# Kernel tuning notes

Hardware: AMD Instinct MI355X
Metric: run time of the kernel (lower is better)

## Reference

```python
import jax, jax.numpy as jnp
import numpy as np

H = 8
D_MODEL = 1024
D_K = D_MODEL // H
NEG = -1000000000.0


def layer_norm(x, a, b, eps=1e-06):
    # torch std: unbiased (ddof=1); module divides by (std + eps)
    mean = jnp.mean(x, axis=-1, keepdims=True)
    var = jnp.sum((x - mean) ** 2, axis=-1, keepdims=True) / (x.shape[-1] - 1)
    std = jnp.sqrt(var)
    return a * (x - mean) / (std + eps) + b


def setup_inputs() -> dict:
    key = jax.random.key(0)
    ks = jax.random.split(key, 12)
    B, S, D = 8, 1024, D_MODEL
    inp = {
        "query": jax.random.normal(ks[0], (B, S, D), jnp.float32),
        "value": jax.random.normal(ks[1], (B, S, D), jnp.float32),
        "key": jax.random.normal(ks[2], (B, S, D), jnp.float32),
        "mask": jax.random.randint(ks[3], (B, S), 0, 2, jnp.int32),
        "ln_a": jnp.ones((D,), jnp.float32),
        "ln_b": jnp.zeros((D,), jnp.float32),
        "wq": jax.random.normal(ks[4], (D, D), jnp.float32) * 0.02,
        "bq": jnp.zeros((D,), jnp.float32),
        "wk": jax.random.normal(ks[5], (D, D), jnp.float32) * 0.02,
        "bk": jnp.zeros((D,), jnp.float32),
        "wv": jax.random.normal(ks[6], (D, D), jnp.float32) * 0.02,
        "bv": jnp.zeros((D,), jnp.float32),
        "w_aoa": jax.random.normal(ks[7], (2 * D, 2 * D), jnp.float32) * 0.02,  # [out, in]
        "b_aoa": jnp.zeros((2 * D,), jnp.float32),
    }
    return inp


def reference(query, value, key, mask, ln_a, ln_b, wq, bq, wk, bk, wv, bv, w_aoa, b_aoa):
    B, S, D = query.shape
    # mask [B,S] -> [B,1,1,S]
    m = mask[:, None, None, :]
    # norm_q
    q = layer_norm(query, ln_a, ln_b)
    # QKV projections, split heads -> [B,H,S,Dk]
    def split_heads(x):
        return x.reshape(B, -1, H, D_K).transpose(0, 2, 1, 3)
    q_ = split_heads(q @ wq.T + bq)
    k_ = split_heads(key @ wk.T + bk)
    v_ = split_heads(value @ wv.T + bv)
    scores = jnp.einsum("bhqd,bhkd->bhqk", q_, k_) / jnp.sqrt(jnp.float32(D_K))
    scores = jnp.where(m == 0, NEG, scores)
    p = jax.nn.softmax(scores, axis=-1)
    x = jnp.einsum("bhqk,bhkd->bhqd", p, v_)
    x = x.transpose(0, 2, 1, 3).reshape(B, S, D)
    # AoA: concat with (normed) query, linear to 2D, GLU
    z = jnp.concatenate([x, q], axis=-1) @ w_aoa.T + b_aoa
    a, g = jnp.split(z, 2, axis=-1)
    return a * jax.nn.sigmoid(g)
```

## Files before the change

### kernel.cpp

```cpp
#include <hip/hip_runtime.h>

typedef __attribute__((ext_vector_type(8))) __bf16 bf16x8;
typedef __attribute__((ext_vector_type(4))) float f32x4;

__device__ __forceinline__ ushort f2b(float f) {
    uint u = __builtin_bit_cast(uint, f);
    u += 0x7fffu + ((u >> 16) & 1u);
    return (ushort)(u >> 16);
}
__device__ __forceinline__ float b2f(ushort h) {
    uint u = ((uint)h) << 16;
    return __builtin_bit_cast(float, u);
}

__global__ __launch_bounds__(256) void cast_kernel(const float* __restrict__ src,
                                                   ushort* __restrict__ dst) {
    size_t i = ((size_t)blockIdx.x * 256 + threadIdx.x) * 4;
    float4 v = *(const float4*)(src + i);
    ushort4 o;
    o.x = f2b(v.x); o.y = f2b(v.y); o.z = f2b(v.z); o.w = f2b(v.w);
    *(ushort4*)(dst + i) = o;
}

__global__ __launch_bounds__(256) void ln_kernel(const float* __restrict__ x,
                                                 const float* __restrict__ ga,
                                                 const float* __restrict__ be,
                                                 ushort* __restrict__ xq) {
    const int row = blockIdx.x, tid = threadIdx.x;
    __shared__ float red[4];
    float4 v = ((const float4*)(x + (size_t)row * 1024))[tid];
    float sm = v.x + v.y + v.z + v.w;
    for (int off = 32; off; off >>= 1) sm += __shfl_xor(sm, off);
    if ((tid & 63) == 0) red[tid >> 6] = sm;
    __syncthreads();
    float mean = (red[0] + red[1] + red[2] + red[3]) * (1.f / 1024.f);
    __syncthreads();
    float dx = v.x - mean, dy = v.y - mean, dz = v.z - mean, dw = v.w - mean;
    float s2 = dx * dx + dy * dy + dz * dz + dw * dw;
    for (int off = 32; off; off >>= 1) s2 += __shfl_xor(s2, off);
    if ((tid & 63) == 0) red[tid >> 6] = s2;
    __syncthreads();
    float var = (red[0] + red[1] + red[2] + red[3]) * (1.f / 1023.f);
    float inv = 1.f / (sqrtf(var) + 1e-6f);
    float4 g = ((const float4*)ga)[tid];
    float4 bb = ((const float4*)be)[tid];
    ushort4 o;
    o.x = f2b(g.x * dx * inv + bb.x);
    o.y = f2b(g.y * dy * inv + bb.y);
    o.z = f2b(g.z * dz * inv + bb.z);
    o.w = f2b(g.w * dw * inv + bb.w);
    *(ushort4*)&xq[(size_t)row * 2048 + 1024 + tid * 4] = o;
}

__global__ __launch_bounds__(256) void gemm2(const ushort* __restrict__ A, int lda,
                                             const ushort* __restrict__ B, int ldb,
                                             const float* __restrict__ bias,
                                             ushort* __restrict__ C, int ldc,
                                             int K, int NB, float scale, int mode) {
    __shared__ ushort As[2][8192];
    __shared__ ushort Bs[2][8192];
    const int tid = threadIdx.x;
    const int w = tid >> 6, l = tid & 63;
    const int wr = w >> 1, wc = w & 1;
    const int r16 = l & 15, g4 = l >> 4;

    const int bid = blockIdx.x;
    const int cpx = gridDim.x >> 3;
    const int swz = (bid & 7) * cpx + (bid >> 3);
    const int m0 = (swz / NB) * 128;
    const int n0 = (swz % NB) * 128;

    const int srow = l >> 3;
    const int scol = ((l & 7) ^ srow) * 8;
    const ushort* Asrc = A + (size_t)(m0 + w * 8 + srow) * lda + scol;
    const ushort* Bsrc = B + (size_t)(n0 + w * 8 + srow) * ldb + scol;

    f32x4 acc[4][4];
#pragma unroll
    for (int i = 0; i < 4; i++)
#pragma unroll
        for (int j = 0; j < 4; j++) acc[i][j] = (f32x4){0.f, 0.f, 0.f, 0.f};

    auto STAGE = [&](int sel, int kt) {
#pragma unroll
        for (int it = 0; it < 4; it++) {
            __builtin_amdgcn_global_load_lds(
                (const __attribute__((address_space(1))) void*)(Asrc + (size_t)(it * 32) * lda + kt * 64),
                (__attribute__((address_space(3))) void*)(&As[sel][(it * 4 + w) * 512]), 16, 0, 0);
            __builtin_amdgcn_global_load_lds(
                (const __attribute__((address_space(1))) void*)(Bsrc + (size_t)(it * 32) * ldb + kt * 64),
                (__attribute__((address_space(3))) void*)(&Bs[sel][(it * 4 + w) * 512]), 16, 0, 0);
        }
    };

    const int swzr = (g4 ^ (r16 & 7)) << 4;

    auto COMPUTE = [&](int sel, int kt, bool stage_next) {
        if (stage_next) STAGE(sel ^ 1, kt + 1);
        const char* Ab = (const char*)&As[sel][0];
        const char* Bb = (const char*)&Bs[sel][0];
        bf16x8 af[4][2], bfv[4][2];
#pragma unroll
        for (int mi = 0; mi < 4; mi++) {
            int ba = (wr * 64 + mi * 16 + r16) * 128 + swzr;
            af[mi][0] = *(const bf16x8*)(Ab + ba);
            af[mi][1] = *(const bf16x8*)(Ab + (ba ^ 64));
        }
#pragma unroll
        for (int ni = 0; ni < 4; ni++) {
            int bb = (wc * 64 + ni * 16 + r16) * 128 + swzr;
            bfv[ni][0] = *(const bf16x8*)(Bb + bb);
            bfv[ni][1] = *(const bf16x8*)(Bb + (bb ^ 64));
        }
        __builtin_amdgcn_s_setprio(1);
#pragma unroll
        for (int ks = 0; ks < 2; ks++)
#pragma unroll
            for (int mi = 0; mi < 4; mi++)
#pragma unroll
                for (int ni = 0; ni < 4; ni++)
                    acc[mi][ni] = __builtin_amdgcn_mfma_f32_16x16x32_bf16(af[mi][ks], bfv[ni][ks], acc[mi][ni], 0, 0, 0);
        __builtin_amdgcn_s_setprio(0);
        asm volatile("s_waitcnt vmcnt(0)" ::: "memory");
        __syncthreads();
    };

    STAGE(0, 0);
    asm volatile("s_waitcnt vmcnt(0)" ::: "memory");
    __syncthreads();
    const int NT = K >> 6;
    for (int kt = 0; kt < NT; kt += 2) {
        COMPUTE(0, kt, true);
        COMPUTE(1, kt + 1, kt + 2 < NT);
    }

    const int row0 = m0 + wr * 64;
    const int col0 = n0 + wc * 64;
    if (mode == 0) {
#pragma unroll
        for (int ni = 0; ni < 4; ni++) {
            int n = col0 + ni * 16 + r16;
            float bs = bias[n];
#pragma unroll
            for (int mi = 0; mi < 4; mi++) {
                int mr = row0 + mi * 16 + g4 * 4;
#pragma unroll
                for (int r = 0; r < 4; r++) {
                    C[(size_t)(mr + r) * ldc + n] = f2b((acc[mi][ni][r] + bs) * scale);
                }
            }
        }
    } else {
#pragma unroll
        for (int ni = 0; ni < 4; ni++) {
            int n = col0 + ni * 16 + r16;
            float bs = bias[n];
            int h = n >> 7, d = n & 127;
#pragma unroll
            for (int mi = 0; mi < 4; mi++) {
                int m = row0 + mi * 16 + g4 * 4;
                int b_ = m >> 10, s_ = m & 1023;
                ushort4 o;
                o.x = f2b((acc[mi][ni][0] + bs) * scale);
                o.y = f2b((acc[mi][ni][1] + bs) * scale);
                o.z = f2b((acc[mi][ni][2] + bs) * scale);
                o.w = f2b((acc[mi][ni][3] + bs) * scale);
                *(ushort4*)&C[((size_t)(b_ * 8 + h) * 128 + d) * 1024 + s_] = o;
            }
        }
    }
}

__global__ __launch_bounds__(512, 2) void gemm3(const ushort* __restrict__ A, int lda,
                                                const ushort* __restrict__ B, int ldb,
                                                const float* __restrict__ bias,
                                                ushort* __restrict__ C, int ldc,
                                                int K, int NB) {
    __shared__ ushort lds[2][32768];

    const int tid = threadIdx.x;
    const int w = tid >> 6, l = tid & 63;
    const int wr = w >> 2, wcn = w & 3;
    const int r16 = l & 15, g4 = l >> 4;

    const int bid = blockIdx.x;
    const int cpx = gridDim.x >> 3;
    const int swz = (bid & 7) * cpx + (bid >> 3);
    const int m0 = (swz / NB) * 256;
    const int n0 = (swz % NB) * 256;

    const int srow8 = l >> 3;
    const int sxor8 = ((l & 7) ^ srow8) * 8;
    const ushort* As0 = A + (size_t)(m0 + w * 8 + srow8) * lda + sxor8;
    const ushort* Bs0 = B + (size_t)(n0 + w * 8 + srow8) * ldb + sxor8;

    f32x4 acc[8][4];
#pragma unroll
    for (int i = 0; i < 8; i++)
#pragma unroll
        for (int j = 0; j < 4; j++) acc[i][j] = (f32x4){0.f, 0.f, 0.f, 0.f};

    const int sw16 = (r16 & 7) << 4;
    char* ldsb = (char*)&lds[0][0];

#define STAGE_H(sel_, HS_, kt_)                                                            \
    do {                                                                                   \
        const int mat_ = (HS_)&1, half_ = (HS_) >> 1;                                      \
        const ushort* sb_ = mat_ ? Bs0 : As0;                                              \
        const int ld_ = mat_ ? ldb : lda;                                                  \
        _Pragma("unroll") for (int li_ = 0; li_ < 2; li_++) {                              \
            const ushort* src_ = sb_ + (size_t)(half_ * 128 + li_ * 64) * ld_ + (kt_)*64;  \
            int dst_ = (sel_)*65536 + mat_ * 32768 + half_ * 16384 + li_ * 8192 + w * 1024;\
            __builtin_amdgcn_global_load_lds(                                              \
                (const __attribute__((address_space(1))) void*)src_,                       \
                (__attribute__((address_space(3))) void*)(ldsb + dst_), 16, 0, 0);         \
        }                                                                                  \
    } while (0)

#define RD_A(sel_, a_, ks_)                                                                  \
    (*(const bf16x8*)(ldsb + (sel_)*65536 + ((a_) >> 2) * 16384 +                            \
                      (wr * 16 + 32 * ((a_)&3) + r16) * 128 + (((ks_)*64 + g4 * 16) ^ sw16)))
#define RD_B(sel_, b_, ks_)                                                                  \
    (*(const bf16x8*)(ldsb + (sel_)*65536 + 32768 + ((b_) >> 1) * 16384 +                    \
                      (wcn * 16 + 64 * ((b_)&1) + r16) * 128 + (((ks_)*64 + g4 * 16) ^ sw16)))

    const int NT = K >> 6;

    STAGE_H(0, 0, 0); STAGE_H(0, 1, 0); STAGE_H(0, 2, 0); STAGE_H(0, 3, 0);
    asm volatile("s_waitcnt vmcnt(0)" ::: "memory");
    __builtin_amdgcn_s_barrier();

    bf16x8 afr[4][2], bfr[2][2];

#define PHASE(sel_, t_, A0_, B0_, RDA_, RDB_, HS_)                                          \
    do {                                                                                    \
        if (RDA_) {                                                                         \
            _Pragma("unroll") for (int ai_ = 0; ai_ < 4; ai_++)                             \
                _Pragma("unroll") for (int ks_ = 0; ks_ < 2; ks_++)                         \
                    afr[ai_][ks_] = RD_A(sel_, (A0_) + ai_, ks_);                           \
        }                                                                                   \
        if (RDB_) {                                                                         \
            _Pragma("unroll") for (int bi_ = 0; bi_ < 2; bi_++)                             \
                _Pragma("unroll") for (int ks_ = 0; ks_ < 2; ks_++)                         \
                    bfr[bi_][ks_] = RD_B(sel_, (B0_) + bi_, ks_);                           \
        }                                                                                   \
        if ((t_) + 1 < NT) STAGE_H((sel_) ^ 1, HS_, (t_) + 1);                              \
        __builtin_amdgcn_s_barrier();                                                       \
        __builtin_amdgcn_s_setprio(1);                                                      \
        _Pragma("unroll") for (int ks_ = 0; ks_ < 2; ks_++)                                 \
            _Pragma("unroll") for (int ai_ = 0; ai_ < 4; ai_++)                             \
                _Pragma("unroll") for (int bi_ = 0; bi_ < 2; bi_++)                         \
                    acc[(A0_) + ai_][(B0_) + bi_] = __builtin_amdgcn_mfma_f32_16x16x32_bf16(\
                        afr[ai_][ks_], bfr[bi_][ks_], acc[(A0_) + ai_][(B0_) + bi_], 0, 0, 0);\
        __builtin_amdgcn_s_setprio(0);                                                      \
        asm volatile("s_waitcnt vmcnt(4)" ::: "memory");                                    \
        __builtin_amdgcn_s_barrier();                                                       \
    } while (0)

    for (int t = 0; t < NT; ++t) {
        const int sel = t & 1;
        PHASE(sel, t, 0, 0, 1, 1, 0);
        PHASE(sel, t, 4, 0, 1, 0, 1);
        PHASE(sel, t, 4, 2, 0, 1, 2);
        PHASE(sel, t, 0, 2, 1, 0, 3);
    }
#undef PHASE
#undef RD_A
#undef RD_B
#undef STAGE_H

#pragma unroll
    for (int b_ = 0; b_ < 4; b_++) {
        int n = n0 + wcn * 16 + 64 * b_ + r16;
        float bs = bias[n];
#pragma unroll
        for (int a_ = 0; a_ < 8; a_++) {
            int mr = m0 + wr * 16 + 32 * a_ + g4 * 4;
#pragma unroll
            for (int r = 0; r < 4; r++) {
                C[(size_t)(mr + r) * ldc + n] = f2b(acc[a_][b_][r] + bs);
            }
        }
    }
}

__global__ __launch_bounds__(512, 4) void attn_kernel(const ushort* __restrict__ Q,
                                                      const ushort* __restrict__ Kt,
                                                      const ushort* __restrict__ Vt,
                                                      const int* __restrict__ mask,
                                                      ushort* __restrict__ xq) {
    __shared__ ushort Ks[2][8192];
    __shared__ ushort Vs[2][8192];
    __shared__ ushort Pl[8][1024];

    const int tid = threadIdx.x;
    const int l = tid & 63, wid = tid >> 6;
    const int r16 = l & 15, g4 = l >> 4;
    const int id = blockIdx.x;
    const int bh = ((id >> 6) << 3) | (id & 7);
    const int qb = (id >> 3) & 7;
    const int b = bh >> 3, h = bh & 7;
    const int q0 = qb * 128 + wid * 16;

    bf16x8 qf[4];
    const ushort* Qrow = Q + (size_t)(b * 1024 + q0 + r16) * 1024 + h * 128 + g4 * 8;
#pragma unroll
    for (int kf = 0; kf < 4; kf++) qf[kf] = *(const bf16x8*)(Qrow + kf * 32);

    const ushort* Kg = Kt + ((size_t)b * 1024) * 1024 + h * 128;
    const ushort* Vg = Vt + (size_t)(b * 8 + h) * 128 * 1024;
    const int* mptr = mask + b * 1024;
    int mv = mptr[l];

    f32x4 xacc[8];
#pragma unroll
    for (int i = 0; i < 8; i++) xacc[i] = (f32x4){0.f, 0.f, 0.f, 0.f};
    float mrow = -INFINITY, lrow = 0.f;

    char* Pme = (char*)&Pl[wid][0];
    const int pswz = (r16 & 7) << 4;

    auto STAGE = [&](int sel, int t) {
        const int kv0 = t * 64;
#pragma unroll
        for (int it = 0; it < 2; ++it) {
            int ob = it * 8192 + wid * 1024;
            int o = ob + l * 16;
            int row = o >> 8;
            int sc = (o & 255) ^ ((row & 7) << 4);
            const ushort* src = Kg + (size_t)(kv0 + row) * 1024 + (sc >> 1);
            __builtin_amdgcn_global_load_lds((const __attribute__((address_space(1))) void*)src,
                (__attribute__((address_space(3))) void*)((char*)&Ks[sel][0] + ob), 16, 0, 0);
        }
#pragma unroll
        for (int it = 0; it < 2; ++it) {
            int ob = it * 8192 + wid * 1024;
            int o = ob + l * 16;
            int d = o >> 7;
            int sc = (o & 127) ^ ((d & 7) << 4);
            const ushort* src = Vg + (size_t)d * 1024 + kv0 + (sc >> 1);
            __builtin_amdgcn_global_load_lds((const __attribute__((address_space(1))) void*)src,
                (__attribute__((address_space(3))) void*)((char*)&Vs[sel][0] + ob), 16, 0, 0);
        }
    };

    STAGE(0, 0);
    int cur = 0;

    for (int t = 0; t < 16; ++t) {
        int mvn = (t < 15) ? mptr[(t + 1) * 64 + l] : 0;
        unsigned long long wt = __ballot(mv != 0);

        asm volatile("s_waitcnt vmcnt(0)" ::: "memory");
        __syncthreads();
        if (t < 15) STAGE(cur ^ 1, t + 1);

        const char* Kb_ = (const char*)&Ks[cur][0];
        const char* Vb_ = (const char*)&Vs[cur][0];

        f32x4 s[4];
#pragma unroll
        for (int cg = 0; cg < 4; cg++) {
            s[cg] = (f32x4){0.f, 0.f, 0.f, 0.f};
            const int rowk = cg * 16 + r16;
            const char* kr = Kb_ + rowk * 256;
            const int sw = (rowk & 7) << 4;
#pragma unroll
            for (int kf = 0; kf < 4; kf++) {
                bf16x8 kfr = *(const bf16x8*)(kr + ((kf * 64 + g4 * 16) ^ sw));
                s[cg] = __builtin_amdgcn_mfma_f32_16x16x32_bf16(kfr, qf[kf], s[cg], 0, 0, 0);
            }
            uint nib = (uint)(wt >> (cg * 16 + g4 * 4)) & 15u;
#pragma unroll
            for (int r = 0; r < 4; r++)
                if (!((nib >> r) & 1u)) s[cg][r] = -1e9f;
        }

        float pmax = -INFINITY;
#pragma unroll
        for (int cg = 0; cg < 4; cg++)
#pragma unroll
            for (int r = 0; r < 4; r++) pmax = fmaxf(pmax, s[cg][r]);
        pmax = fmaxf(pmax, __shfl_xor(pmax, 16));
        pmax = fmaxf(pmax, __shfl_xor(pmax, 32));
        float mn = fmaxf(mrow, pmax);
        float scl = __expf(mrow - mn);
        mrow = mn;

        float rsum = 0.f;
#pragma unroll
        for (int cg = 0; cg < 4; cg++)
#pragma unroll
            for (int r = 0; r < 4; r++) {
                float p = __expf(s[cg][r] - mn);
                s[cg][r] = p;
                rsum += p;
            }
        rsum += __shfl_xor(rsum, 16);
        rsum += __shfl_xor(rsum, 32);
        lrow = lrow * scl + rsum;

#pragma unroll
        for (int cg = 0; cg < 4; cg++) {
            uint lo = ((uint)f2b(s[cg][1]) << 16) | f2b(s[cg][0]);
            uint hi = ((uint)f2b(s[cg][3]) << 16) | f2b(s[cg][2]);
            uint2 pk; pk.x = lo; pk.y = hi;
            *(uint2*)(Pme + r16 * 128 + ((cg * 32 + g4 * 8) ^ pswz)) = pk;
        }

#pragma unroll
        for (int cg2 = 0; cg2 < 8; cg2++)
#pragma unroll
            for (int r = 0; r < 4; r++) xacc[cg2][r] *= scl;

#pragma unroll
        for (int ks = 0; ks < 2; ks++) {
            bf16x8 pfr = *(const bf16x8*)(Pme + r16 * 128 + ((g4 * 16 + ks * 64) ^ pswz));
#pragma unroll
            for (int cg2 = 0; cg2 < 8; cg2++) {
                const int d = cg2 * 16 + r16;
                bf16x8 vfr = *(const bf16x8*)(Vb_ + d * 128 + ((ks * 64 + g4 * 16) ^ ((d & 7) << 4)));
                xacc[cg2] = __builtin_amdgcn_mfma_f32_16x16x32_bf16(vfr, pfr, xacc[cg2], 0, 0, 0);
            }
        }
        mv = mvn;
        cur ^= 1;
    }

    const float inv = 1.f / lrow;
    const size_t orow = (size_t)(b * 1024 + q0 + r16) * 2048 + h * 128;
#pragma unroll
    for (int cg2 = 0; cg2 < 8; cg2++) {
#pragma unroll
        for (int r = 0; r < 4; r++) {
            xq[orow + cg2 * 16 + g4 * 4 + r] = f2b(xacc[cg2][r] * inv);
        }
    }
}

__global__ __launch_bounds__(256) void glu_kernel(const ushort* __restrict__ z,
                                                  float* __restrict__ out) {
    size_t i = (size_t)blockIdx.x * 1024 + (size_t)threadIdx.x * 4;
    size_t row = i >> 10;
    int c = (int)(i & 1023);
    ushort4 av = *(const ushort4*)&z[row * 2048 + c];
    ushort4 gv = *(const ushort4*)&z[row * 2048 + 1024 + c];
    float4 o;
    o.x = b2f(av.x) * (1.f / (1.f + __expf(-b2f(gv.x))));
    o.y = b2f(av.y) * (1.f / (1.f + __expf(-b2f(gv.y))));
    o.z = b2f(av.z) * (1.f / (1.f + __expf(-b2f(gv.z))));
    o.w = b2f(av.w) * (1.f / (1.f + __expf(-b2f(gv.w))));
    *(float4*)&out[i] = o;
}

extern "C" void kernel_launch(void* const* d_in, const int* in_sizes, int n_in,
                              void* d_out, int out_size, void* d_ws, size_t ws_size,
                              hipStream_t stream) {
    const float* query = (const float*)d_in[0];
    const float* value = (const float*)d_in[1];
    const float* key   = (const float*)d_in[2];
    const int*   mask  = (const int*)d_in[3];
    const float* ln_a  = (const float*)d_in[4];
    const float* ln_b  = (const float*)d_in[5];
    const float* wq    = (const float*)d_in[6];
    const float* bq    = (const float*)d_in[7];
    const float* wk    = (const float*)d_in[8];
    const float* bk    = (const float*)d_in[9];
    const float* wv    = (const float*)d_in[10];
    const float* bv    = (const float*)d_in[11];
    const float* waoa  = (const float*)d_in[12];
    const float* baoa  = (const float*)d_in[13];
    float* out = (float*)d_out;

    char* w8 = (char*)d_ws;
    ushort* xq   = (ushort*)(w8);
    ushort* Qb   = (ushort*)(w8 + 33554432);
    ushort* Kb   = (ushort*)(w8 + 50331648);
    ushort* Vt   = (ushort*)(w8 + 67108864);
    ushort* keyb = (ushort*)(w8 + 83886080);
    ushort* valb = (ushort*)(w8 + 100663296);
    ushort* zb   = (ushort*)(w8 + 83886080);
    ushort* wqb  = (ushort*)(w8 + 117440512);
    ushort* wkb  = (ushort*)(w8 + 119537664);
    ushort* wvb  = (ushort*)(w8 + 121634816);
    ushort* wab  = (ushort*)(w8 + 123731968);

    cast_kernel<<<8192, 256, 0, stream>>>(key, keyb);
    cast_kernel<<<8192, 256, 0, stream>>>(value, valb);
    cast_kernel<<<1024, 256, 0, stream>>>(wq, wqb);
    cast_kernel<<<1024, 256, 0, stream>>>(wk, wkb);
    cast_kernel<<<1024, 256, 0, stream>>>(wv, wvb);
    cast_kernel<<<4096, 256, 0, stream>>>(waoa, wab);
    ln_kernel<<<8192, 256, 0, stream>>>(query, ln_a, ln_b, xq);

    const float qscale = 0.08838834764831845f;
    gemm2<<<512, 256, 0, stream>>>(xq + 1024, 2048, wqb, 1024, bq, Qb, 1024, 1024, 8, qscale, 0);
    gemm2<<<512, 256, 0, stream>>>(keyb, 1024, wkb, 1024, bk, Kb, 1024, 1024, 8, 1.f, 0);
    gemm2<<<512, 256, 0, stream>>>(valb, 1024, wvb, 1024, bv, Vt, 0, 1024, 8, 1.f, 1);

    attn_kernel<<<512, 512, 0, stream>>>(Qb, Kb, Vt, mask, xq);

    gemm3<<<256, 512, 0, stream>>>(xq, 2048, wab, 2048, baoa, zb, 2048, 2048, 8);
    glu_kernel<<<8192, 256, 0, stream>>>(zb, out);
}
```

Measured before the change: 266.9 us.

## Fuse GLU into AoA GEMM epilogue and software-pipeline attention QK/PV

```diff
diff --git a/kernel.cpp b/kernel.cpp
--- a/kernel.cpp
+++ b/kernel.cpp
@@ -20,6 +20,17 @@
     ushort4 o;
     o.x = f2b(v.x); o.y = f2b(v.y); o.z = f2b(v.z); o.w = f2b(v.w);
     *(ushort4*)(dst + i) = o;
+}
+
+__global__ __launch_bounds__(256) void cast_permute_aoa(const float* __restrict__ src,
+                                                        ushort* __restrict__ dst) {
+    int n1 = blockIdx.x >> 1;
+    int c = (blockIdx.x & 1) * 1024 + threadIdx.x * 4;
+    int q = ((n1 & 63) | ((n1 >> 7) << 6)) + ((n1 >> 6) & 1) * 1024;
+    float4 v = *(const float4*)(src + (size_t)q * 2048 + c);
+    ushort4 o;
+    o.x = f2b(v.x); o.y = f2b(v.y); o.z = f2b(v.z); o.w = f2b(v.w);
+    *(ushort4*)(dst + (size_t)n1 * 2048 + c) = o;
 }
 
 __global__ __launch_bounds__(256) void ln_kernel(const float* __restrict__ x,
@@ -174,7 +185,7 @@
 __global__ __launch_bounds__(512, 2) void gemm3(const ushort* __restrict__ A, int lda,
                                                 const ushort* __restrict__ B, int ldb,
                                                 const float* __restrict__ bias,
-                                                ushort* __restrict__ C, int ldc,
+                                                float* __restrict__ out,
                                                 int K, int NB) {
     __shared__ ushort lds[2][32768];
 
@@ -217,12 +228,36 @@
         }                                                                                  \
     } while (0)
 
-#define RD_A(sel_, a_, ks_)                                                                  \
-    (*(const bf16x8*)(ldsb + (sel_)*65536 + ((a_) >> 2) * 16384 +                            \
-                      (wr * 16 + 32 * ((a_)&3) + r16) * 128 + (((ks_)*64 + g4 * 16) ^ sw16)))
-#define RD_B(sel_, b_, ks_)                                                                  \
-    (*(const bf16x8*)(ldsb + (sel_)*65536 + 32768 + ((b_) >> 1) * 16384 +                    \
-                      (wcn * 16 + 64 * ((b_)&1) + r16) * 128 + (((ks_)*64 + g4 * 16) ^ sw16)))
+    auto LDA4 = [&](bf16x8 (&dst)[4][2], int sel, int half) {
+#pragma unroll
+        for (int ai = 0; ai < 4; ai++)
+#pragma unroll
+            for (int ks = 0; ks < 2; ks++)
+                dst[ai][ks] = *(const bf16x8*)(ldsb + sel * 65536 + half * 16384 +
+                                               (wr * 16 + 32 * ai + r16) * 128 +
+                                               ((ks * 64 + g4 * 16) ^ sw16));
+    };
+    auto LDB2 = [&](bf16x8 (&dst)[2][2], int sel, int half) {
+#pragma unroll
+        for (int bi = 0; bi < 2; bi++)
+#pragma unroll
+            for (int ks = 0; ks < 2; ks++)
+                dst[bi][ks] = *(const bf16x8*)(ldsb + sel * 65536 + 32768 + half * 16384 +
+                                               (wcn * 16 + 64 * bi + r16) * 128 +
+                                               ((ks * 64 + g4 * 16) ^ sw16));
+    };
+    auto MM = [&](bf16x8 (&af)[4][2], bf16x8 (&bf)[2][2], int A0, int B0) {
+        __builtin_amdgcn_s_setprio(1);
+#pragma unroll
+        for (int ks = 0; ks < 2; ks++)
+#pragma unroll
+            for (int ai = 0; ai < 4; ai++)
+#pragma unroll
+                for (int bi = 0; bi < 2; bi++)
+                    acc[A0 + ai][B0 + bi] = __builtin_amdgcn_mfma_f32_16x16x32_bf16(
+                        af[ai][ks], bf[bi][ks], acc[A0 + ai][B0 + bi], 0, 0, 0);
+        __builtin_amdgcn_s_setprio(0);
+    };
 
     const int NT = K >> 6;
 
@@ -230,55 +265,50 @@
     asm volatile("s_waitcnt vmcnt(0)" ::: "memory");
     __builtin_amdgcn_s_barrier();
 
-    bf16x8 afr[4][2], bfr[2][2];
-
-#define PHASE(sel_, t_, A0_, B0_, RDA_, RDB_, HS_)                                          \
-    do {                                                                                    \
-        if (RDA_) {                                                                         \
-            _Pragma("unroll") for (int ai_ = 0; ai_ < 4; ai_++)                             \
-                _Pragma("unroll") for (int ks_ = 0; ks_ < 2; ks_++)                         \
-                    afr[ai_][ks_] = RD_A(sel_, (A0_) + ai_, ks_);                           \
-        }                                                                                   \
-        if (RDB_) {                                                                         \
-            _Pragma("unroll") for (int bi_ = 0; bi_ < 2; bi_++)                             \
-                _Pragma("unroll") for (int ks_ = 0; ks_ < 2; ks_++)                         \
-                    bfr[bi_][ks_] = RD_B(sel_, (B0_) + bi_, ks_);                           \
-        }                                                                                   \
-        if ((t_) + 1 < NT) STAGE_H((sel_) ^ 1, HS_, (t_) + 1);                              \
-        __builtin_amdgcn_s_barrier();                                                       \
-        __builtin_amdgcn_s_setprio(1);                                                      \
-        _Pragma("unroll") for (int ks_ = 0; ks_ < 2; ks_++)                                 \
-            _Pragma("unroll") for (int ai_ = 0; ai_ < 4; ai_++)                             \
-                _Pragma("unroll") for (int bi_ = 0; bi_ < 2; bi_++)                         \
-                    acc[(A0_) + ai_][(B0_) + bi_] = __builtin_amdgcn_mfma_f32_16x16x32_bf16(\
-                        afr[ai_][ks_], bfr[bi_][ks_], acc[(A0_) + ai_][(B0_) + bi_], 0, 0, 0);\
-        __builtin_amdgcn_s_setprio(0);                                                      \
-        asm volatile("s_waitcnt vmcnt(4)" ::: "memory");                                    \
-        __builtin_amdgcn_s_barrier();                                                       \
-    } while (0)
+    bf16x8 aL[4][2], aH[4][2], bL[2][2], bH[2][2];
 
     for (int t = 0; t < NT; ++t) {
         const int sel = t & 1;
-        PHASE(sel, t, 0, 0, 1, 1, 0);
-        PHASE(sel, t, 4, 0, 1, 0, 1);
-        PHASE(sel, t, 4, 2, 0, 1, 2);
-        PHASE(sel, t, 0, 2, 1, 0, 3);
-    }
-#undef PHASE
-#undef RD_A
-#undef RD_B
+        const bool pf = (t + 1 < NT);
+        LDA4(aL, sel, 0); LDB2(bL, sel, 0);
+        if (pf) STAGE_H(sel ^ 1, 0, t + 1);
+        __builtin_amdgcn_s_barrier();
+        MM(aL, bL, 0, 0);
+        asm volatile("s_waitcnt vmcnt(4)" ::: "memory");
+        __builtin_amdgcn_s_barrier();
+        LDA4(aH, sel, 1);
+        if (pf) STAGE_H(sel ^ 1, 1, t + 1);
+        __builtin_amdgcn_s_barrier();
+        MM(aH, bL, 4, 0);
+        asm volatile("s_waitcnt vmcnt(4)" ::: "memory");
+        __builtin_amdgcn_s_barrier();
+        LDB2(bH, sel, 1);
+        if (pf) STAGE_H(sel ^ 1, 2, t + 1);
+        __builtin_amdgcn_s_barrier();
+        MM(aH, bH, 4, 2);
+        asm volatile("s_waitcnt vmcnt(4)" ::: "memory");
+        __builtin_amdgcn_s_barrier();
+        if (pf) STAGE_H(sel ^ 1, 3, t + 1);
+        __builtin_amdgcn_s_barrier();
+        MM(aL, bH, 0, 2);
+        asm volatile("s_waitcnt vmcnt(4)" ::: "memory");
+        __builtin_amdgcn_s_barrier();
+    }
 #undef STAGE_H
 
 #pragma unroll
-    for (int b_ = 0; b_ < 4; b_++) {
-        int n = n0 + wcn * 16 + 64 * b_ + r16;
-        float bs = bias[n];
+    for (int bp = 0; bp < 2; bp++) {
+        int j = (n0 >> 1) + wcn * 16 + 64 * bp + r16;
+        float bsa = bias[j];
+        float bsg = bias[j + 1024];
 #pragma unroll
         for (int a_ = 0; a_ < 8; a_++) {
             int mr = m0 + wr * 16 + 32 * a_ + g4 * 4;
 #pragma unroll
             for (int r = 0; r < 4; r++) {
-                C[(size_t)(mr + r) * ldc + n] = f2b(acc[a_][b_][r] + bs);
+                float av = acc[a_][2 * bp][r] + bsa;
+                float gv = acc[a_][2 * bp + 1][r] + bsg;
+                out[(size_t)(mr + r) * 1024 + j] = av * (1.f / (1.f + __expf(-gv)));
             }
         }
     }
@@ -310,17 +340,16 @@
     const ushort* Kg = Kt + ((size_t)b * 1024) * 1024 + h * 128;
     const ushort* Vg = Vt + (size_t)(b * 8 + h) * 128 * 1024;
     const int* mptr = mask + b * 1024;
-    int mv = mptr[l];
 
     f32x4 xacc[8];
 #pragma unroll
     for (int i = 0; i < 8; i++) xacc[i] = (f32x4){0.f, 0.f, 0.f, 0.f};
-    float mrow = -INFINITY, lrow = 0.f;
+    float mrow = -INFINITY, lrow = 0.f, sclp = 0.f;
 
     char* Pme = (char*)&Pl[wid][0];
     const int pswz = (r16 & 7) << 4;
 
-    auto STAGE = [&](int sel, int t) {
+    auto STAGE_K = [&](int sel, int t) {
         const int kv0 = t * 64;
 #pragma unroll
         for (int it = 0; it < 2; ++it) {
@@ -332,6 +361,9 @@
             __builtin_amdgcn_global_load_lds((const __attribute__((address_space(1))) void*)src,
                 (__attribute__((address_space(3))) void*)((char*)&Ks[sel][0] + ob), 16, 0, 0);
         }
+    };
+    auto STAGE_V = [&](int sel, int t) {
+        const int kv0 = t * 64;
 #pragma unroll
         for (int it = 0; it < 2; ++it) {
             int ob = it * 8192 + wid * 1024;
@@ -344,38 +376,50 @@
         }
     };
 
-    STAGE(0, 0);
-    int cur = 0;
-
-    for (int t = 0; t < 16; ++t) {
-        int mvn = (t < 15) ? mptr[(t + 1) * 64 + l] : 0;
-        unsigned long long wt = __ballot(mv != 0);
-
-        asm volatile("s_waitcnt vmcnt(0)" ::: "memory");
-        __syncthreads();
-        if (t < 15) STAGE(cur ^ 1, t + 1);
-
-        const char* Kb_ = (const char*)&Ks[cur][0];
-        const char* Vb_ = (const char*)&Vs[cur][0];
-
-        f32x4 s[4];
+    auto QK = [&](f32x4 (&s)[4], int sel, unsigned long long wt) {
+        const char* Kb_ = (const char*)&Ks[sel][0];
 #pragma unroll
         for (int cg = 0; cg < 4; cg++) {
             s[cg] = (f32x4){0.f, 0.f, 0.f, 0.f};
             const int rowk = cg * 16 + r16;
             const char* kr = Kb_ + rowk * 256;
             const int sw = (rowk & 7) << 4;
+            __builtin_amdgcn_s_setprio(1);
 #pragma unroll
             for (int kf = 0; kf < 4; kf++) {
                 bf16x8 kfr = *(const bf16x8*)(kr + ((kf * 64 + g4 * 16) ^ sw));
                 s[cg] = __builtin_amdgcn_mfma_f32_16x16x32_bf16(kfr, qf[kf], s[cg], 0, 0, 0);
             }
+            __builtin_amdgcn_s_setprio(0);
             uint nib = (uint)(wt >> (cg * 16 + g4 * 4)) & 15u;
 #pragma unroll
             for (int r = 0; r < 4; r++)
                 if (!((nib >> r) & 1u)) s[cg][r] = -1e9f;
         }
-
+    };
+    auto PV = [&](int sel) {
+        const char* Vb_ = (const char*)&Vs[sel][0];
+        bf16x8 pfr[2];
+#pragma unroll
+        for (int ks = 0; ks < 2; ks++)
+            pfr[ks] = *(const bf16x8*)(Pme + r16 * 128 + ((g4 * 16 + ks * 64) ^ pswz));
+#pragma unroll
+        for (int cg2 = 0; cg2 < 8; cg2++)
+#pragma unroll
+            for (int r = 0; r < 4; r++) xacc[cg2][r] *= sclp;
+        __builtin_amdgcn_s_setprio(1);
+#pragma unroll
+        for (int ks = 0; ks < 2; ks++) {
+#pragma unroll
+            for (int cg2 = 0; cg2 < 8; cg2++) {
+                const int d = cg2 * 16 + r16;
+                bf16x8 vfr = *(const bf16x8*)(Vb_ + d * 128 + ((ks * 64 + g4 * 16) ^ ((d & 7) << 4)));
+                xacc[cg2] = __builtin_amdgcn_mfma_f32_16x16x32_bf16(vfr, pfr[ks], xacc[cg2], 0, 0, 0);
+            }
+        }
+        __builtin_amdgcn_s_setprio(0);
+    };
+    auto SOFTMAX = [&](f32x4 (&s)[4]) {
         float pmax = -INFINITY;
 #pragma unroll
         for (int cg = 0; cg < 4; cg++)
@@ -384,9 +428,8 @@
         pmax = fmaxf(pmax, __shfl_xor(pmax, 16));
         pmax = fmaxf(pmax, __shfl_xor(pmax, 32));
         float mn = fmaxf(mrow, pmax);
-        float scl = __expf(mrow - mn);
+        sclp = __expf(mrow - mn);
         mrow = mn;
-
         float rsum = 0.f;
 #pragma unroll
         for (int cg = 0; cg < 4; cg++)
@@ -398,8 +441,7 @@
             }
         rsum += __shfl_xor(rsum, 16);
         rsum += __shfl_xor(rsum, 32);
-        lrow = lrow * scl + rsum;
-
+        lrow = lrow * sclp + rsum;
 #pragma unroll
         for (int cg = 0; cg < 4; cg++) {
             uint lo = ((uint)f2b(s[cg][1]) << 16) | f2b(s[cg][0]);
@@ -407,25 +449,42 @@
             uint2 pk; pk.x = lo; pk.y = hi;
             *(uint2*)(Pme + r16 * 128 + ((cg * 32 + g4 * 8) ^ pswz)) = pk;
         }
-
-#pragma unroll
-        for (int cg2 = 0; cg2 < 8; cg2++)
-#pragma unroll
-            for (int r = 0; r < 4; r++) xacc[cg2][r] *= scl;
-
-#pragma unroll
-        for (int ks = 0; ks < 2; ks++) {
-            bf16x8 pfr = *(const bf16x8*)(Pme + r16 * 128 + ((g4 * 16 + ks * 64) ^ pswz));
-#pragma unroll
-            for (int cg2 = 0; cg2 < 8; cg2++) {
-                const int d = cg2 * 16 + r16;
-                bf16x8 vfr = *(const bf16x8*)(Vb_ + d * 128 + ((ks * 64 + g4 * 16) ^ ((d & 7) << 4)));
-                xacc[cg2] = __builtin_amdgcn_mfma_f32_16x16x32_bf16(vfr, pfr, xacc[cg2], 0, 0, 0);
-            }
-        }
-        mv = mvn;
-        cur ^= 1;
-    }
+    };
+
+    STAGE_K(0, 0);
+    int mv = mptr[l];
+    asm volatile("s_waitcnt vmcnt(0)" ::: "memory");
+    __syncthreads();
+    STAGE_K(1, 1);
+    STAGE_V(0, 0);
+    unsigned long long wt = __ballot(mv != 0);
+    mv = mptr[64 + l];
+    {
+        f32x4 s0[4];
+        QK(s0, 0, wt);
+        SOFTMAX(s0);
+    }
+    int kc = 1, vc = 0;
+
+    for (int u = 1; u < 16; ++u) {
+        wt = __ballot(mv != 0);
+        asm volatile("s_waitcnt vmcnt(0)" ::: "memory");
+        __syncthreads();
+        if (u < 15) STAGE_K(kc ^ 1, u + 1);
+        STAGE_V(vc ^ 1, u);
+        if (u < 15) mv = mptr[(u + 1) * 64 + l];
+
+        f32x4 sn[4];
+        QK(sn, kc, wt);
+        PV(vc);
+        SOFTMAX(sn);
+
+        kc ^= 1; vc ^= 1;
+    }
+
+    asm volatile("s_waitcnt vmcnt(0)" ::: "memory");
+    __syncthreads();
+    PV(vc);
 
     const float inv = 1.f / lrow;
     const size_t orow = (size_t)(b * 1024 + q0 + r16) * 2048 + h * 128;
@@ -436,21 +495,6 @@
             xq[orow + cg2 * 16 + g4 * 4 + r] = f2b(xacc[cg2][r] * inv);
         }
     }
-}
-
-__global__ __launch_bounds__(256) void glu_kernel(const ushort* __restrict__ z,
-                                                  float* __restrict__ out) {
-    size_t i = (size_t)blockIdx.x * 1024 + (size_t)threadIdx.x * 4;
-    size_t row = i >> 10;
-    int c = (int)(i & 1023);
-    ushort4 av = *(const ushort4*)&z[row * 2048 + c];
-    ushort4 gv = *(const ushort4*)&z[row * 2048 + 1024 + c];
-    float4 o;
-    o.x = b2f(av.x) * (1.f / (1.f + __expf(-b2f(gv.x))));
-    o.y = b2f(av.y) * (1.f / (1.f + __expf(-b2f(gv.y))));
-    o.z = b2f(av.z) * (1.f / (1.f + __expf(-b2f(gv.z))));
-    o.w = b2f(av.w) * (1.f / (1.f + __expf(-b2f(gv.w))));
-    *(float4*)&out[i] = o;
 }
 
 extern "C" void kernel_launch(void* const* d_in, const int* in_sizes, int n_in,
@@ -479,7 +523,6 @@
     ushort* Vt   = (ushort*)(w8 + 67108864);
     ushort* keyb = (ushort*)(w8 + 83886080);
     ushort* valb = (ushort*)(w8 + 100663296);
-    ushort* zb   = (ushort*)(w8 + 83886080);
     ushort* wqb  = (ushort*)(w8 + 117440512);
     ushort* wkb  = (ushort*)(w8 + 119537664);
     ushort* wvb  = (ushort*)(w8 + 121634816);
@@ -490,7 +533,7 @@
     cast_kernel<<<1024, 256, 0, stream>>>(wq, wqb);
     cast_kernel<<<1024, 256, 0, stream>>>(wk, wkb);
     cast_kernel<<<1024, 256, 0, stream>>>(wv, wvb);
-    cast_kernel<<<4096, 256, 0, stream>>>(waoa, wab);
+    cast_permute_aoa<<<4096, 256, 0, stream>>>(waoa, wab);
     ln_kernel<<<8192, 256, 0, stream>>>(query, ln_a, ln_b, xq);
 
     const float qscale = 0.08838834764831845f;
@@ -500,6 +543,5 @@
 
     attn_kernel<<<512, 512, 0, stream>>>(Qb, Kb, Vt, mask, xq);
 
-    gemm3<<<256, 512, 0, stream>>>(xq, 2048, wab, 2048, baoa, zb, 2048, 2048, 8);
-    glu_kernel<<<8192, 256, 0, stream>>>(zb, out);
-}
+    gemm3<<<256, 512, 0, stream>>>(xq, 2048, wab, 2048, baoa, out, 2048, 8);
+}
```

Measured after the change: 242.6 us. 1.1x faster.
